# Optimization experiments

Hardware: AMD Instinct MI355X
Metric: run time of the kernel (lower is better)

The kernel has to match this reference:

```python
import jax, jax.numpy as jnp
import numpy as np

TEMPERATURE = 0.5
LAMBDA_REG = 0.1
NUM_GROUPS = 4  # number of distinct sensitive-attribute values
EPS = 1e-8      # torch cosine_similarity norm clamp


def setup_inputs() -> dict:
    key = jax.random.key(0)
    k1, k2, k3 = jax.random.split(key, 3)
    B, D = 4096, 256
    return {
        "z_i": jax.random.normal(k1, (B, D), dtype=jnp.float32),
        "z_j": jax.random.normal(k2, (B, D), dtype=jnp.float32),
        "sensitive_features": jax.random.randint(k3, (B,), 0, NUM_GROUPS, dtype=jnp.int64),
    }


def reference(z_i, z_j, sensitive_features):
    B = z_i.shape[0]
    z = jnp.concatenate([z_i, z_j], axis=0)                       # [2B, D]
    norm = jnp.maximum(jnp.linalg.norm(z, axis=1, keepdims=True), EPS)
    zn = z / norm                                                  # row-normalized
    S = zn @ zn.T                                                  # [2B, 2B] cosine sims

    # NT-Xent contrastive term
    pos = jnp.concatenate([jnp.diagonal(S, offset=B), jnp.diagonal(S, offset=-B)])  # [2B]
    mask = 1.0 - jnp.eye(2 * B, dtype=S.dtype)                     # zero out self-sims
    den = jnp.sum(mask * jnp.exp(S / TEMPERATURE), axis=1)         # [2B]
    contrastive = jnp.sum(-(pos / TEMPERATURE) + jnp.log(den)) / (2 * B)

    # Fairness penalty over groups of the FIRST B rows (indices come from sensitive_features)
    Sg = S[:B, :B]
    onehot = jax.nn.one_hot(sensitive_features, NUM_GROUPS, dtype=S.dtype)  # [B, G]
    group_sums = jnp.sum(onehot * (Sg @ onehot), axis=0)           # [G] sum_{i,j in g} S[i,j] (incl. diag, as torch)
    counts = jnp.sum(onehot, axis=0)                               # [G]
    per_group = jnp.where(counts > 1, group_sums / (counts * (counts - 1.0)), 0.0)
    num_unique = jnp.sum(counts > 0).astype(S.dtype)
    fairness = LAMBDA_REG * (jnp.sum(per_group) / num_unique)

    return contrastive + fairness
```

## Files before the change

### kernel.cpp

```cpp
#include <hip/hip_runtime.h>
#include <hip/hip_bf16.h>

typedef __attribute__((ext_vector_type(8))) short short8;
typedef __attribute__((ext_vector_type(4))) float f32x4;
typedef __attribute__((address_space(1))) const void gvoid_t;
typedef __attribute__((address_space(3))) void lvoid_t;

#define NB 4096
#define DD 256
#define TWOB 8192
#define NMACRO 1056u
#define GSUM_BLOCKS 16
#define NPART 1072u

__device__ __forceinline__ unsigned short f2bf(float f) {
  unsigned int u = __float_as_uint(f);
  u += 0x7fffu + ((u >> 16) & 1u);
  return (unsigned short)(u >> 16);
}
__device__ __forceinline__ float bf2f(unsigned short s) {
  return __uint_as_float(((unsigned int)s) << 16);
}


__global__ __launch_bounds__(256) void norm_kernel(const float* __restrict__ zi,
                                                   const float* __restrict__ zj,
                                                   float* __restrict__ wsf,
                                                   float* __restrict__ ppos,
                                                   unsigned short* __restrict__ znb) {
  __shared__ float sred[4];
  if (blockIdx.x < 32) wsf[blockIdx.x * 256 + threadIdx.x] = 0.f;
  const int lane = threadIdx.x & 63, wave = threadIdx.x >> 6;
  const int i = blockIdx.x * 4 + wave;

  float4 a = ((const float4*)(zi + (size_t)i * DD))[lane];
  float4 b = ((const float4*)(zj + (size_t)i * DD))[lane];
  float sa = a.x * a.x + a.y * a.y + a.z * a.z + a.w * a.w;
  float sb = b.x * b.x + b.y * b.y + b.z * b.z + b.w * b.w;
  float sab = a.x * b.x + a.y * b.y + a.z * b.z + a.w * b.w;
#pragma unroll
  for (int m = 32; m >= 1; m >>= 1) {
    sa += __shfl_xor(sa, m);
    sb += __shfl_xor(sb, m);
    sab += __shfl_xor(sab, m);
  }
  float ra = 1.0f / fmaxf(sqrtf(sa), 1e-8f);
  float rb = 1.0f / fmaxf(sqrtf(sb), 1e-8f);
  ushort4 oa, ob;
  oa.x = f2bf(a.x * ra); oa.y = f2bf(a.y * ra); oa.z = f2bf(a.z * ra); oa.w = f2bf(a.w * ra);
  ob.x = f2bf(b.x * rb); ob.y = f2bf(b.y * rb); ob.z = f2bf(b.z * rb); ob.w = f2bf(b.w * rb);
  ((ushort4*)(znb + (size_t)i * DD))[lane] = oa;
  ((ushort4*)(znb + (size_t)(i + NB) * DD))[lane] = ob;

  if (lane == 0) sred[wave] = sab * ra * rb;
  __syncthreads();
  if (threadIdx.x == 0)
    ppos[blockIdx.x] = sred[0] + sred[1] + sred[2] + sred[3];
}

__global__ __launch_bounds__(512, 4) void den_kernel(const int* __restrict__ sf,
                                                     float* __restrict__ wsf,
                                                     const unsigned short* __restrict__ znb,
                                                     float* __restrict__ vsum_part,
                                                     int* __restrict__ cnt_part) {
  __shared__ __align__(16) unsigned short As[3][4096];
  __shared__ __align__(16) unsigned short Bs[3][8192];

  float* den = wsf;

  const int tid = threadIdx.x;
  const int lane = tid & 63, wave = tid >> 6;
  const unsigned t_raw = blockIdx.y * 64u + blockIdx.x;
  if (t_raw >= NPART) return;
  const unsigned t_lin = (t_raw & 7u) * 134u + (t_raw >> 3);

  if (t_lin < GSUM_BLOCKS) {
    const int b = (int)t_lin;
    const int r0 = b * 256;
    float acc[4][4];
#pragma unroll
    for (int q = 0; q < 4; ++q)
#pragma unroll
      for (int e = 0; e < 4; ++e) acc[q][e] = 0.f;
    int cnt[4] = {0, 0, 0, 0};
    const int rw = r0 + wave * 32;
    for (int k = 0; k < 32; ++k) {
      int row = rw + k;
      int g = sf[row];
      ushort4 v = ((const ushort4*)(znb + (size_t)row * DD))[lane];
      float f0 = bf2f(v.x), f1 = bf2f(v.y), f2 = bf2f(v.z), f3 = bf2f(v.w);
#pragma unroll
      for (int q = 0; q < 4; ++q) {
        bool sel = (g == q);
        acc[q][0] += sel ? f0 : 0.f;
        acc[q][1] += sel ? f1 : 0.f;
        acc[q][2] += sel ? f2 : 0.f;
        acc[q][3] += sel ? f3 : 0.f;
        cnt[q] += sel ? 1 : 0;
      }
    }
    float4* lsd = (float4*)&Bs[0][0];
    int* lcnt = (int*)&As[0][0];
#pragma unroll
    for (int q = 0; q < 4; ++q) {
      float4 t;
      t.x = acc[q][0]; t.y = acc[q][1]; t.z = acc[q][2]; t.w = acc[q][3];
      lsd[(wave * 4 + q) * 64 + lane] = t;
    }
    if (lane == 0) {
#pragma unroll
      for (int q = 0; q < 4; ++q) lcnt[wave * 4 + q] = cnt[q];
    }
    __syncthreads();
    if (tid < 256) {
      int g = tid >> 6, l = tid & 63;
      float4 s = {0.f, 0.f, 0.f, 0.f};
#pragma unroll
      for (int w = 0; w < 8; ++w) {
        float4 sv = lsd[(w * 4 + g) * 64 + l];
        s.x += sv.x; s.y += sv.y; s.z += sv.z; s.w += sv.w;
      }
      ((float4*)(vsum_part + (size_t)(b * 4 + g) * 256))[l] = s;
      if (tid < 4) {
        int ci = 0;
#pragma unroll
        for (int w = 0; w < 8; ++w) ci += lcnt[w * 4 + tid];
        cnt_part[b * 4 + tid] = ci;
      }
    }
    return;
  }

  unsigned t = t_lin - GSUM_BLOCKS;
  unsigned tr = 0;
  while (t >= 32u - (tr >> 1)) { t -= 32u - (tr >> 1); ++tr; }
  unsigned c = (tr >> 1) + t;
  const size_t rowbase = (size_t)tr * 128;
  const size_t colbase = (size_t)c * 256;

  const int u = lane >> 3;
  const int cp = (lane & 7) ^ u;
  const int ri = 2 * u + (cp >> 2);
  const int kelem = (cp & 3) * 8;
  const int slot = ((((lane & 1) << 2) | (lane >> 4)) ^ ((lane >> 1) & 7));
  const int fragoff = ((lane & 15) >> 1) * 128 + slot * 16;
  const int wrow = wave & 1;
  const int wcol = wave >> 1;

  const int tch = (int)(2 * c) + (wcol >> 1);
  const float fr = (tch >= (int)tr) ? 1.f : 0.f;
  const float fc = (tch > (int)tr) ? 1.f : 0.f;

  f32x4 zero = {0.f, 0.f, 0.f, 0.f};
  f32x4 acc[4][4];
#pragma unroll
  for (int i = 0; i < 4; ++i)
#pragma unroll
    for (int j = 0; j < 4; ++j) acc[i][j] = zero;

  const unsigned short* gA = znb + (rowbase + wave * 16 + ri) * DD + kelem;
  const unsigned short* gB0 = znb + (colbase + (2 * wave) * 16 + ri) * DD + kelem;
  const unsigned short* gB1 = gB0 + 16 * DD;

  auto stage = [&](int kt, int buf) {
    __builtin_amdgcn_global_load_lds((gvoid_t*)(gA + kt * 32), (lvoid_t*)&As[buf][wave * 512], 16, 0, 0);
    __builtin_amdgcn_global_load_lds((gvoid_t*)(gB0 + kt * 32), (lvoid_t*)&Bs[buf][(2 * wave) * 512], 16, 0, 0);
    __builtin_amdgcn_global_load_lds((gvoid_t*)(gB1 + kt * 32), (lvoid_t*)&Bs[buf][(2 * wave + 1) * 512], 16, 0, 0);
  };

  stage(0, 0);
  stage(1, 1);
#pragma unroll
  for (int kt = 0; kt < 8; ++kt) {
    const int buf = kt % 3;
    if (kt < 7) asm volatile("s_waitcnt vmcnt(3)" ::: "memory");
    else        asm volatile("s_waitcnt vmcnt(0)" ::: "memory");
    __builtin_amdgcn_s_barrier();
    asm volatile("" ::: "memory");
    if (kt < 6) stage(kt + 2, (kt + 2) % 3);
    short8 af[4], bfr[4];
#pragma unroll
    for (int mi = 0; mi < 4; ++mi)
      af[mi] = *(const short8*)((const char*)&As[0][0] + buf * 8192 + (wrow * 4 + mi) * 1024 + fragoff);
#pragma unroll
    for (int ni = 0; ni < 4; ++ni)
      bfr[ni] = *(const short8*)((const char*)&Bs[0][0] + buf * 16384 + (wcol * 4 + ni) * 1024 + fragoff);
#pragma unroll
    for (int mi = 0; mi < 4; ++mi)
#pragma unroll
      for (int ni = 0; ni < 4; ++ni)
        acc[mi][ni] = __builtin_amdgcn_mfma_f32_16x16x32_bf16(af[mi], bfr[ni], acc[mi][ni], 0, 0, 0);
  }

  float rsum[4][4];
  float csum[4];
#pragma unroll
  for (int mi = 0; mi < 4; ++mi)
#pragma unroll
    for (int r = 0; r < 4; ++r) rsum[mi][r] = 0.f;
#pragma unroll
  for (int ni = 0; ni < 4; ++ni) csum[ni] = 0.f;
#pragma unroll
  for (int mi = 0; mi < 4; ++mi)
#pragma unroll
    for (int ni = 0; ni < 4; ++ni)
#pragma unroll
      for (int r = 0; r < 4; ++r) {
        float e = __expf(2.0f * acc[mi][ni][r]);
        rsum[mi][r] += e;
        csum[ni] += e;
      }
#pragma unroll
  for (int m = 1; m < 16; m <<= 1)
#pragma unroll
    for (int mi = 0; mi < 4; ++mi)
#pragma unroll
      for (int r = 0; r < 4; ++r) rsum[mi][r] += __shfl_xor(rsum[mi][r], m);
#pragma unroll
  for (int m = 16; m < 64; m <<= 1)
#pragma unroll
    for (int ni = 0; ni < 4; ++ni) csum[ni] += __shfl_xor(csum[ni], m);

  float* Lr = (float*)&As[0][0];
  float* Lc = Lr + 512;
  if ((lane & 15) == 0) {
    int h = lane >> 4;
#pragma unroll
    for (int mi = 0; mi < 4; ++mi)
#pragma unroll
      for (int r = 0; r < 4; ++r)
        Lr[wcol * 128 + wrow * 64 + mi * 16 + h * 4 + r] = rsum[mi][r] * fr;
  }
  if (lane < 16) {
#pragma unroll
    for (int ni = 0; ni < 4; ++ni)
      Lc[wrow * 256 + wcol * 64 + ni * 16 + lane] = csum[ni] * fc;
  }
  __syncthreads();
  if (tid < 256) {
    float v = Lc[tid] + Lc[256 + tid];
    if (v != 0.f) unsafeAtomicAdd(&den[colbase + tid], v);
  } else if (tid < 384) {
    int r = tid - 256;
    unsafeAtomicAdd(&den[rowbase + r], Lr[r] + Lr[128 + r] + Lr[256 + r] + Lr[384 + r]);
  }
}

__global__ __launch_bounds__(1024) void tail_kernel(const float* __restrict__ wsf,
                                                    const float* __restrict__ vsum_part,
                                                    const int* __restrict__ cnt_part,
                                                    const float* __restrict__ ppos,
                                                    float* __restrict__ out) {
  __shared__ float sred[48];
  const float* den = wsf;
  const int tid = threadIdx.x;
  const int lane = tid & 63, wave = tid >> 6;

  const float e2 = __expf(2.0f);
  float ls = 0.f;
#pragma unroll
  for (int k = 0; k < 8; ++k) ls += __logf(den[k * 1024 + tid] - e2);
#pragma unroll
  for (int m = 32; m >= 1; m >>= 1) ls += __shfl_xor(ls, m);
  if (lane == 0) sred[wave] = ls;

  float pp = ppos[tid];
#pragma unroll
  for (int m = 32; m >= 1; m >>= 1) pp += __shfl_xor(pp, m);
  if (lane == 0) sred[16 + wave] = pp;

  {
    int g = tid >> 8, col = tid & 255;
    float v = 0.f;
#pragma unroll
    for (int b = 0; b < 16; ++b) v += vsum_part[(size_t)(b * 4 + g) * 256 + col];
    float gp = v * v;
#pragma unroll
    for (int m = 32; m >= 1; m >>= 1) gp += __shfl_xor(gp, m);
    if (lane == 0) sred[32 + wave] = gp;
  }
  __syncthreads();
  if (tid == 0) {
    float lsum = 0.f, psum = 0.f;
#pragma unroll
    for (int w = 0; w < 16; ++w) { lsum += sred[w]; psum += sred[16 + w]; }
    float contrastive = (lsum - 4.0f * psum) / (float)TWOB;
    float fsum = 0.f;
    int uniq = 0;
#pragma unroll
    for (int q = 0; q < 4; ++q) {
      int ci = 0;
#pragma unroll
      for (int b = 0; b < 16; ++b) ci += cnt_part[b * 4 + q];
      float gsq = sred[32 + q * 4] + sred[33 + q * 4] + sred[34 + q * 4] + sred[35 + q * 4];
      float cf = (float)ci;
      if (ci > 0) uniq++;
      if (ci > 1) fsum += gsq / (cf * (cf - 1.0f));
    }
    out[0] = contrastive + 0.1f * (fsum / (uniq > 0 ? (float)uniq : 1.0f));
  }
}

extern "C" void kernel_launch(void* const* d_in, const int* in_sizes, int n_in,
                              void* d_out, int out_size, void* d_ws, size_t ws_size,
                              hipStream_t stream) {
  const float* zi = (const float*)d_in[0];
  const float* zj = (const float*)d_in[1];
  const int* sf = (const int*)d_in[2];
  float* out = (float*)d_out;
  char* ws = (char*)d_ws;
  float* wsf = (float*)ws;
  unsigned short* znb = (unsigned short*)(ws + 65536);
  float* vsum_part = (float*)(ws + 4259840);
  int* cnt_part = (int*)(ws + 4276224);
  float* ppos = (float*)(ws + 4276480);

  hipLaunchKernelGGL(norm_kernel, dim3(1024), dim3(256), 0, stream, zi, zj, wsf, ppos, znb);
  hipLaunchKernelGGL(den_kernel, dim3(64, 17), dim3(512), 0, stream,
                     sf, wsf, znb, vsum_part, cnt_part);
  hipLaunchKernelGGL(tail_kernel, dim3(1), dim3(1024), 0, stream,
                     wsf, vsum_part, cnt_part, ppos, out);
}
```

Baseline: 96.65 us.

## Switch similarity kernel to 128x128 symmetric tiles with 256-thread blocks

Reshapes the upper-triangular similarity tiling from 128x256 macro tiles with 512-thread blocks to square 128x128 tiles with 256-thread blocks. Tiles are enumerated directly over the triangle, which removes the half-tile masking factors. Diagonal tiles skip the column atomics. The group-sum blocks are adjusted to use 4 waves. This doubles the block count and shrinks LDS per block to improve scheduling and load balance, at the cost of less operand reuse per tile and more atomics overall.

```diff
diff --git a/kernel.cpp b/kernel.cpp
--- a/kernel.cpp
+++ b/kernel.cpp
@@ -9,9 +9,9 @@
 #define NB 4096
 #define DD 256
 #define TWOB 8192
-#define NMACRO 1056u
+#define NMACRO 2080u
 #define GSUM_BLOCKS 16
-#define NPART 1072u
+#define NPART 2096u
 
 __device__ __forceinline__ unsigned short f2bf(float f) {
   unsigned int u = __float_as_uint(f);
@@ -58,13 +58,13 @@
     ppos[blockIdx.x] = sred[0] + sred[1] + sred[2] + sred[3];
 }
 
-__global__ __launch_bounds__(512, 4) void den_kernel(const int* __restrict__ sf,
+__global__ __launch_bounds__(256, 3) void den_kernel(const int* __restrict__ sf,
                                                      float* __restrict__ wsf,
                                                      const unsigned short* __restrict__ znb,
                                                      float* __restrict__ vsum_part,
                                                      int* __restrict__ cnt_part) {
   __shared__ __align__(16) unsigned short As[3][4096];
-  __shared__ __align__(16) unsigned short Bs[3][8192];
+  __shared__ __align__(16) unsigned short Bs[3][4096];
 
   float* den = wsf;
 
@@ -72,7 +72,7 @@
   const int lane = tid & 63, wave = tid >> 6;
   const unsigned t_raw = blockIdx.y * 64u + blockIdx.x;
   if (t_raw >= NPART) return;
-  const unsigned t_lin = (t_raw & 7u) * 134u + (t_raw >> 3);
+  const unsigned t_lin = (t_raw & 7u) * 262u + (t_raw >> 3);
 
   if (t_lin < GSUM_BLOCKS) {
     const int b = (int)t_lin;
@@ -83,8 +83,8 @@
 #pragma unroll
       for (int e = 0; e < 4; ++e) acc[q][e] = 0.f;
     int cnt[4] = {0, 0, 0, 0};
-    const int rw = r0 + wave * 32;
-    for (int k = 0; k < 32; ++k) {
+    const int rw = r0 + wave * 64;
+    for (int k = 0; k < 64; ++k) {
       int row = rw + k;
       int g = sf[row];
       ushort4 v = ((const ushort4*)(znb + (size_t)row * DD))[lane];
@@ -99,8 +99,8 @@
         cnt[q] += sel ? 1 : 0;
       }
     }
-    float4* lsd = (float4*)&Bs[0][0];
-    int* lcnt = (int*)&As[0][0];
+    float4* lsd = (float4*)&As[0][0];
+    int* lcnt = (int*)&Bs[0][0];
 #pragma unroll
     for (int q = 0; q < 4; ++q) {
       float4 t;
@@ -112,31 +112,31 @@
       for (int q = 0; q < 4; ++q) lcnt[wave * 4 + q] = cnt[q];
     }
     __syncthreads();
-    if (tid < 256) {
+    {
       int g = tid >> 6, l = tid & 63;
-      float4 s = {0.f, 0.f, 0.f, 0.f};
-#pragma unroll
-      for (int w = 0; w < 8; ++w) {
-        float4 sv = lsd[(w * 4 + g) * 64 + l];
-        s.x += sv.x; s.y += sv.y; s.z += sv.z; s.w += sv.w;
-      }
+      float4 s0 = lsd[(0 + g) * 64 + l];
+      float4 s1 = lsd[(4 + g) * 64 + l];
+      float4 s2 = lsd[(8 + g) * 64 + l];
+      float4 s3 = lsd[(12 + g) * 64 + l];
+      float4 s;
+      s.x = s0.x + s1.x + s2.x + s3.x;
+      s.y = s0.y + s1.y + s2.y + s3.y;
+      s.z = s0.z + s1.z + s2.z + s3.z;
+      s.w = s0.w + s1.w + s2.w + s3.w;
       ((float4*)(vsum_part + (size_t)(b * 4 + g) * 256))[l] = s;
-      if (tid < 4) {
-        int ci = 0;
-#pragma unroll
-        for (int w = 0; w < 8; ++w) ci += lcnt[w * 4 + tid];
-        cnt_part[b * 4 + tid] = ci;
-      }
+      if (tid < 4)
+        cnt_part[b * 4 + tid] = lcnt[tid] + lcnt[4 + tid] + lcnt[8 + tid] + lcnt[12 + tid];
     }
     return;
   }
 
   unsigned t = t_lin - GSUM_BLOCKS;
-  unsigned tr = 0;
-  while (t >= 32u - (tr >> 1)) { t -= 32u - (tr >> 1); ++tr; }
-  unsigned c = (tr >> 1) + t;
-  const size_t rowbase = (size_t)tr * 128;
-  const size_t colbase = (size_t)c * 256;
+  unsigned i = 0;
+  while (t >= 64u - i) { t -= 64u - i; ++i; }
+  unsigned j = i + t;
+  const size_t rowbase = (size_t)i * 128;
+  const size_t colbase = (size_t)j * 128;
+  const bool offdiag = (j > i);
 
   const int u = lane >> 3;
   const int cp = (lane & 7) ^ u;
@@ -147,23 +147,21 @@
   const int wrow = wave & 1;
   const int wcol = wave >> 1;
 
-  const int tch = (int)(2 * c) + (wcol >> 1);
-  const float fr = (tch >= (int)tr) ? 1.f : 0.f;
-  const float fc = (tch > (int)tr) ? 1.f : 0.f;
-
   f32x4 zero = {0.f, 0.f, 0.f, 0.f};
   f32x4 acc[4][4];
 #pragma unroll
-  for (int i = 0; i < 4; ++i)
-#pragma unroll
-    for (int j = 0; j < 4; ++j) acc[i][j] = zero;
-
-  const unsigned short* gA = znb + (rowbase + wave * 16 + ri) * DD + kelem;
+  for (int a = 0; a < 4; ++a)
+#pragma unroll
+    for (int b2 = 0; b2 < 4; ++b2) acc[a][b2] = zero;
+
+  const unsigned short* gA0 = znb + (rowbase + (2 * wave) * 16 + ri) * DD + kelem;
+  const unsigned short* gA1 = gA0 + 16 * DD;
   const unsigned short* gB0 = znb + (colbase + (2 * wave) * 16 + ri) * DD + kelem;
   const unsigned short* gB1 = gB0 + 16 * DD;
 
   auto stage = [&](int kt, int buf) {
-    __builtin_amdgcn_global_load_lds((gvoid_t*)(gA + kt * 32), (lvoid_t*)&As[buf][wave * 512], 16, 0, 0);
+    __builtin_amdgcn_global_load_lds((gvoid_t*)(gA0 + kt * 32), (lvoid_t*)&As[buf][(2 * wave) * 512], 16, 0, 0);
+    __builtin_amdgcn_global_load_lds((gvoid_t*)(gA1 + kt * 32), (lvoid_t*)&As[buf][(2 * wave + 1) * 512], 16, 0, 0);
     __builtin_amdgcn_global_load_lds((gvoid_t*)(gB0 + kt * 32), (lvoid_t*)&Bs[buf][(2 * wave) * 512], 16, 0, 0);
     __builtin_amdgcn_global_load_lds((gvoid_t*)(gB1 + kt * 32), (lvoid_t*)&Bs[buf][(2 * wave + 1) * 512], 16, 0, 0);
   };
@@ -173,7 +171,7 @@
 #pragma unroll
   for (int kt = 0; kt < 8; ++kt) {
     const int buf = kt % 3;
-    if (kt < 7) asm volatile("s_waitcnt vmcnt(3)" ::: "memory");
+    if (kt < 7) asm volatile("s_waitcnt vmcnt(4)" ::: "memory");
     else        asm volatile("s_waitcnt vmcnt(0)" ::: "memory");
     __builtin_amdgcn_s_barrier();
     asm volatile("" ::: "memory");
@@ -184,7 +182,7 @@
       af[mi] = *(const short8*)((const char*)&As[0][0] + buf * 8192 + (wrow * 4 + mi) * 1024 + fragoff);
 #pragma unroll
     for (int ni = 0; ni < 4; ++ni)
-      bfr[ni] = *(const short8*)((const char*)&Bs[0][0] + buf * 16384 + (wcol * 4 + ni) * 1024 + fragoff);
+      bfr[ni] = *(const short8*)((const char*)&Bs[0][0] + buf * 8192 + (wcol * 4 + ni) * 1024 + fragoff);
 #pragma unroll
     for (int mi = 0; mi < 4; ++mi)
 #pragma unroll
@@ -222,27 +220,26 @@
     for (int ni = 0; ni < 4; ++ni) csum[ni] += __shfl_xor(csum[ni], m);
 
   float* Lr = (float*)&As[0][0];
-  float* Lc = Lr + 512;
+  float* Lc = Lr + 256;
   if ((lane & 15) == 0) {
     int h = lane >> 4;
 #pragma unroll
     for (int mi = 0; mi < 4; ++mi)
 #pragma unroll
       for (int r = 0; r < 4; ++r)
-        Lr[wcol * 128 + wrow * 64 + mi * 16 + h * 4 + r] = rsum[mi][r] * fr;
+        Lr[wcol * 128 + wrow * 64 + mi * 16 + h * 4 + r] = rsum[mi][r];
   }
   if (lane < 16) {
 #pragma unroll
     for (int ni = 0; ni < 4; ++ni)
-      Lc[wrow * 256 + wcol * 64 + ni * 16 + lane] = csum[ni] * fc;
+      Lc[wrow * 128 + wcol * 64 + ni * 16 + lane] = csum[ni];
   }
   __syncthreads();
-  if (tid < 256) {
-    float v = Lc[tid] + Lc[256 + tid];
-    if (v != 0.f) unsafeAtomicAdd(&den[colbase + tid], v);
-  } else if (tid < 384) {
-    int r = tid - 256;
-    unsafeAtomicAdd(&den[rowbase + r], Lr[r] + Lr[128 + r] + Lr[256 + r] + Lr[384 + r]);
+  if (tid < 128) {
+    unsafeAtomicAdd(&den[rowbase + tid], Lr[tid] + Lr[128 + tid]);
+  } else if (offdiag) {
+    int cc = tid - 128;
+    unsafeAtomicAdd(&den[colbase + cc], Lc[cc] + Lc[128 + cc]);
   }
 }
 
@@ -316,7 +313,7 @@
   float* ppos = (float*)(ws + 4276480);
 
   hipLaunchKernelGGL(norm_kernel, dim3(1024), dim3(256), 0, stream, zi, zj, wsf, ppos, znb);
-  hipLaunchKernelGGL(den_kernel, dim3(64, 17), dim3(512), 0, stream,
+  hipLaunchKernelGGL(den_kernel, dim3(64, 33), dim3(256), 0, stream,
                      sf, wsf, znb, vsum_part, cnt_part);
   hipLaunchKernelGGL(tail_kernel, dim3(1), dim3(1024), 0, stream,
                      wsf, vsum_part, cnt_part, ppos, out);
```

After: 98.51 us. About the same (+1.9%).

## Keep row panel resident in LDS and sweep up to four column tiles per block

Applied to the files above, without the earlier changes.

Reworks the symmetric Gram tiling so each block loads a 128-row A panel once into LDS (all 8 K-slices) and then loops over up to four 128-column B tiles, reusing A across them. Grid shrinks from 1072 to 560 work items, and per-tile row/column exp sums are atomically added, with column sums skipped on diagonal tiles. This is meant to cut redundant A-panel global loads and launch overhead. In exchange it lowers occupancy (launch bounds 4→2, larger LDS footprint), serializes several tiles per block, and uses a smaller 128x128 tile per iteration.

```diff
diff --git a/kernel.cpp b/kernel.cpp
--- a/kernel.cpp
+++ b/kernel.cpp
@@ -9,9 +9,8 @@
 #define NB 4096
 #define DD 256
 #define TWOB 8192
-#define NMACRO 1056u
 #define GSUM_BLOCKS 16
-#define NPART 1072u
+#define NPART 560u
 
 __device__ __forceinline__ unsigned short f2bf(float f) {
   unsigned int u = __float_as_uint(f);
@@ -58,21 +57,21 @@
     ppos[blockIdx.x] = sred[0] + sred[1] + sred[2] + sred[3];
 }
 
-__global__ __launch_bounds__(512, 4) void den_kernel(const int* __restrict__ sf,
+__global__ __launch_bounds__(512, 2) void den_kernel(const int* __restrict__ sf,
                                                      float* __restrict__ wsf,
                                                      const unsigned short* __restrict__ znb,
                                                      float* __restrict__ vsum_part,
                                                      int* __restrict__ cnt_part) {
-  __shared__ __align__(16) unsigned short As[3][4096];
-  __shared__ __align__(16) unsigned short Bs[3][8192];
+  __shared__ __align__(16) unsigned short As8[8][4096];
+  __shared__ __align__(16) unsigned short Bs[3][4096];
+  __shared__ __align__(16) float Scr[768];
 
   float* den = wsf;
 
   const int tid = threadIdx.x;
   const int lane = tid & 63, wave = tid >> 6;
-  const unsigned t_raw = blockIdx.y * 64u + blockIdx.x;
-  if (t_raw >= NPART) return;
-  const unsigned t_lin = (t_raw & 7u) * 134u + (t_raw >> 3);
+  const unsigned t_raw = blockIdx.y * 70u + blockIdx.x;
+  const unsigned t_lin = (t_raw & 7u) * 70u + (t_raw >> 3);
 
   if (t_lin < GSUM_BLOCKS) {
     const int b = (int)t_lin;
@@ -99,8 +98,8 @@
         cnt[q] += sel ? 1 : 0;
       }
     }
-    float4* lsd = (float4*)&Bs[0][0];
-    int* lcnt = (int*)&As[0][0];
+    float4* lsd = (float4*)&As8[0][0];
+    int* lcnt = (int*)&Scr[0];
 #pragma unroll
     for (int q = 0; q < 4; ++q) {
       float4 t;
@@ -132,11 +131,11 @@
   }
 
   unsigned t = t_lin - GSUM_BLOCKS;
-  unsigned tr = 0;
-  while (t >= 32u - (tr >> 1)) { t -= 32u - (tr >> 1); ++tr; }
-  unsigned c = (tr >> 1) + t;
-  const size_t rowbase = (size_t)tr * 128;
-  const size_t colbase = (size_t)c * 256;
+  unsigned i = 0;
+  while (t >= ((67u - i) >> 2)) { t -= (67u - i) >> 2; ++i; }
+  const unsigned j0 = i + 4u * t;
+  const int nt = (int)((64u - j0 < 4u) ? (64u - j0) : 4u);
+  const size_t rowbase = (size_t)i * 128;
 
   const int u = lane >> 3;
   const int cp = (lane & 7) ^ u;
@@ -147,102 +146,114 @@
   const int wrow = wave & 1;
   const int wcol = wave >> 1;
 
-  const int tch = (int)(2 * c) + (wcol >> 1);
-  const float fr = (tch >= (int)tr) ? 1.f : 0.f;
-  const float fc = (tch > (int)tr) ? 1.f : 0.f;
+  const unsigned short* gA = znb + (rowbase + wave * 16 + ri) * DD + kelem;
 
   f32x4 zero = {0.f, 0.f, 0.f, 0.f};
-  f32x4 acc[4][4];
-#pragma unroll
-  for (int i = 0; i < 4; ++i)
-#pragma unroll
-    for (int j = 0; j < 4; ++j) acc[i][j] = zero;
-
-  const unsigned short* gA = znb + (rowbase + wave * 16 + ri) * DD + kelem;
-  const unsigned short* gB0 = znb + (colbase + (2 * wave) * 16 + ri) * DD + kelem;
-  const unsigned short* gB1 = gB0 + 16 * DD;
-
-  auto stage = [&](int kt, int buf) {
-    __builtin_amdgcn_global_load_lds((gvoid_t*)(gA + kt * 32), (lvoid_t*)&As[buf][wave * 512], 16, 0, 0);
-    __builtin_amdgcn_global_load_lds((gvoid_t*)(gB0 + kt * 32), (lvoid_t*)&Bs[buf][(2 * wave) * 512], 16, 0, 0);
-    __builtin_amdgcn_global_load_lds((gvoid_t*)(gB1 + kt * 32), (lvoid_t*)&Bs[buf][(2 * wave + 1) * 512], 16, 0, 0);
-  };
-
-  stage(0, 0);
-  stage(1, 1);
-#pragma unroll
-  for (int kt = 0; kt < 8; ++kt) {
-    const int buf = kt % 3;
-    if (kt < 7) asm volatile("s_waitcnt vmcnt(3)" ::: "memory");
-    else        asm volatile("s_waitcnt vmcnt(0)" ::: "memory");
-    __builtin_amdgcn_s_barrier();
-    asm volatile("" ::: "memory");
-    if (kt < 6) stage(kt + 2, (kt + 2) % 3);
-    short8 af[4], bfr[4];
-#pragma unroll
-    for (int mi = 0; mi < 4; ++mi)
-      af[mi] = *(const short8*)((const char*)&As[0][0] + buf * 8192 + (wrow * 4 + mi) * 1024 + fragoff);
-#pragma unroll
-    for (int ni = 0; ni < 4; ++ni)
-      bfr[ni] = *(const short8*)((const char*)&Bs[0][0] + buf * 16384 + (wcol * 4 + ni) * 1024 + fragoff);
-#pragma unroll
-    for (int mi = 0; mi < 4; ++mi)
-#pragma unroll
-      for (int ni = 0; ni < 4; ++ni)
-        acc[mi][ni] = __builtin_amdgcn_mfma_f32_16x16x32_bf16(af[mi], bfr[ni], acc[mi][ni], 0, 0, 0);
-  }
-
-  float rsum[4][4];
-  float csum[4];
-#pragma unroll
-  for (int mi = 0; mi < 4; ++mi)
-#pragma unroll
-    for (int r = 0; r < 4; ++r) rsum[mi][r] = 0.f;
-#pragma unroll
-  for (int ni = 0; ni < 4; ++ni) csum[ni] = 0.f;
-#pragma unroll
-  for (int mi = 0; mi < 4; ++mi)
-#pragma unroll
-    for (int ni = 0; ni < 4; ++ni)
-#pragma unroll
-      for (int r = 0; r < 4; ++r) {
-        float e = __expf(2.0f * acc[mi][ni][r]);
-        rsum[mi][r] += e;
-        csum[ni] += e;
-      }
-#pragma unroll
-  for (int m = 1; m < 16; m <<= 1)
-#pragma unroll
-    for (int mi = 0; mi < 4; ++mi)
-#pragma unroll
-      for (int r = 0; r < 4; ++r) rsum[mi][r] += __shfl_xor(rsum[mi][r], m);
-#pragma unroll
-  for (int m = 16; m < 64; m <<= 1)
-#pragma unroll
-    for (int ni = 0; ni < 4; ++ni) csum[ni] += __shfl_xor(csum[ni], m);
-
-  float* Lr = (float*)&As[0][0];
-  float* Lc = Lr + 512;
-  if ((lane & 15) == 0) {
-    int h = lane >> 4;
-#pragma unroll
-    for (int mi = 0; mi < 4; ++mi)
-#pragma unroll
-      for (int r = 0; r < 4; ++r)
-        Lr[wcol * 128 + wrow * 64 + mi * 16 + h * 4 + r] = rsum[mi][r] * fr;
-  }
-  if (lane < 16) {
-#pragma unroll
-    for (int ni = 0; ni < 4; ++ni)
-      Lc[wrow * 256 + wcol * 64 + ni * 16 + lane] = csum[ni] * fc;
-  }
-  __syncthreads();
-  if (tid < 256) {
-    float v = Lc[tid] + Lc[256 + tid];
-    if (v != 0.f) unsafeAtomicAdd(&den[colbase + tid], v);
-  } else if (tid < 384) {
-    int r = tid - 256;
-    unsafeAtomicAdd(&den[rowbase + r], Lr[r] + Lr[128 + r] + Lr[256 + r] + Lr[384 + r]);
+  f32x4 acc[4][2];
+
+  for (int tt = 0; tt < nt; ++tt) {
+    const size_t colbase = (size_t)(j0 + tt) * 128;
+    const bool offdiag = (j0 + tt) > i;
+    const unsigned short* gB = znb + (colbase + wave * 16 + ri) * DD + kelem;
+
+#pragma unroll
+    for (int a = 0; a < 4; ++a)
+#pragma unroll
+      for (int b2 = 0; b2 < 2; ++b2) acc[a][b2] = zero;
+
+    if (tt == 0) {
+      __builtin_amdgcn_global_load_lds((gvoid_t*)(gA + 0 * 32), (lvoid_t*)&As8[0][wave * 512], 16, 0, 0);
+      __builtin_amdgcn_global_load_lds((gvoid_t*)(gB + 0 * 32), (lvoid_t*)&Bs[0][wave * 512], 16, 0, 0);
+      __builtin_amdgcn_global_load_lds((gvoid_t*)(gA + 1 * 32), (lvoid_t*)&As8[1][wave * 512], 16, 0, 0);
+      __builtin_amdgcn_global_load_lds((gvoid_t*)(gB + 1 * 32), (lvoid_t*)&Bs[1][wave * 512], 16, 0, 0);
+    } else {
+      __builtin_amdgcn_global_load_lds((gvoid_t*)(gB + 0 * 32), (lvoid_t*)&Bs[0][wave * 512], 16, 0, 0);
+      __builtin_amdgcn_global_load_lds((gvoid_t*)(gB + 1 * 32), (lvoid_t*)&Bs[1][wave * 512], 16, 0, 0);
+    }
+
+#pragma unroll
+    for (int kt = 0; kt < 8; ++kt) {
+      if (kt < 7) asm volatile("s_waitcnt vmcnt(1)" ::: "memory");
+      else        asm volatile("s_waitcnt vmcnt(0)" ::: "memory");
+      __builtin_amdgcn_s_barrier();
+      asm volatile("" ::: "memory");
+      if (kt < 6) {
+        if (tt == 0)
+          __builtin_amdgcn_global_load_lds((gvoid_t*)(gA + (kt + 2) * 32),
+                                           (lvoid_t*)&As8[kt + 2][wave * 512], 16, 0, 0);
+        __builtin_amdgcn_global_load_lds((gvoid_t*)(gB + (kt + 2) * 32),
+                                         (lvoid_t*)&Bs[(kt + 2) % 3][wave * 512], 16, 0, 0);
+      }
+      short8 af[4], bfr[2];
+#pragma unroll
+      for (int mi = 0; mi < 4; ++mi)
+        af[mi] = *(const short8*)((const char*)&As8[0][0] + kt * 8192 + (wrow * 4 + mi) * 1024 + fragoff);
+#pragma unroll
+      for (int ni = 0; ni < 2; ++ni)
+        bfr[ni] = *(const short8*)((const char*)&Bs[0][0] + (kt % 3) * 8192 + (wcol * 2 + ni) * 1024 + fragoff);
+#pragma unroll
+      for (int mi = 0; mi < 4; ++mi)
+#pragma unroll
+        for (int ni = 0; ni < 2; ++ni)
+          acc[mi][ni] = __builtin_amdgcn_mfma_f32_16x16x32_bf16(af[mi], bfr[ni], acc[mi][ni], 0, 0, 0);
+    }
+
+    {
+      float rsum[4][4];
+      float csum[2];
+#pragma unroll
+      for (int mi = 0; mi < 4; ++mi)
+#pragma unroll
+        for (int r = 0; r < 4; ++r) rsum[mi][r] = 0.f;
+#pragma unroll
+      for (int ni = 0; ni < 2; ++ni) csum[ni] = 0.f;
+#pragma unroll
+      for (int mi = 0; mi < 4; ++mi)
+#pragma unroll
+        for (int ni = 0; ni < 2; ++ni)
+#pragma unroll
+          for (int r = 0; r < 4; ++r) {
+            float e = __expf(2.0f * acc[mi][ni][r]);
+            rsum[mi][r] += e;
+            csum[ni] += e;
+          }
+#pragma unroll
+      for (int m = 1; m < 16; m <<= 1)
+#pragma unroll
+        for (int mi = 0; mi < 4; ++mi)
+#pragma unroll
+          for (int r = 0; r < 4; ++r) rsum[mi][r] += __shfl_xor(rsum[mi][r], m);
+#pragma unroll
+      for (int m = 16; m < 64; m <<= 1)
+#pragma unroll
+        for (int ni = 0; ni < 2; ++ni) csum[ni] += __shfl_xor(csum[ni], m);
+
+      float* Lr = &Scr[0];
+      float* Lc = &Scr[512];
+      if ((lane & 15) == 0) {
+        int h = lane >> 4;
+#pragma unroll
+        for (int mi = 0; mi < 4; ++mi)
+#pragma unroll
+          for (int r = 0; r < 4; ++r)
+            Lr[wcol * 128 + wrow * 64 + mi * 16 + h * 4 + r] = rsum[mi][r];
+      }
+      if (lane < 16) {
+#pragma unroll
+        for (int ni = 0; ni < 2; ++ni)
+          Lc[wrow * 128 + wcol * 32 + ni * 16 + lane] = csum[ni];
+      }
+      asm volatile("s_waitcnt lgkmcnt(0)" ::: "memory");
+      __builtin_amdgcn_s_barrier();
+      asm volatile("" ::: "memory");
+      if (tid < 128) {
+        unsafeAtomicAdd(&den[rowbase + tid],
+                        Lr[tid] + Lr[128 + tid] + Lr[256 + tid] + Lr[384 + tid]);
+      } else if (offdiag && tid < 256) {
+        int cc = tid - 128;
+        unsafeAtomicAdd(&den[colbase + cc], Lc[cc] + Lc[128 + cc]);
+      }
+    }
   }
 }
 
@@ -316,7 +327,7 @@
   float* ppos = (float*)(ws + 4276480);
 
   hipLaunchKernelGGL(norm_kernel, dim3(1024), dim3(256), 0, stream, zi, zj, wsf, ppos, znb);
-  hipLaunchKernelGGL(den_kernel, dim3(64, 17), dim3(512), 0, stream,
+  hipLaunchKernelGGL(den_kernel, dim3(70, 8), dim3(512), 0, stream,
                      sf, wsf, znb, vsum_part, cnt_part);
   hipLaunchKernelGGL(tail_kernel, dim3(1), dim3(1024), 0, stream,
                      wsf, vsum_part, cnt_part, ppos, out);
```

Result: slower. 120.5 us (+24.6%).
